# Optimization experiments

Measured on AMD Instinct MI355X. Metric: run time of the kernel, lower is better.

The kernel has to match this reference:

```python
import jax, jax.numpy as jnp
import numpy as np

B, S = 256, 16384
HUBER_DELTA = 1.0  # torch.nn.HuberLoss default


def setup_inputs() -> dict:
    key = jax.random.key(0)
    k1, k2, k3 = jax.random.split(key, 3)
    pred_coords = jax.random.normal(k1, (B, S, 3), dtype=jnp.float32)
    target_coords = jax.random.normal(k2, (B, S, 3), dtype=jnp.float32)
    mask = jax.random.randint(k3, (B, S), 0, 2).astype(jnp.int32)
    return {"pred_coords": pred_coords, "target_coords": target_coords, "mask": mask}


def _kabsch_align(pred, target, maskf):
    # pred/target: [B,S,3], maskf: [B,S] (0/1). Batched masked Kabsch.
    cnt = maskf.sum(axis=1, keepdims=True)                      # [B,1]
    cp = (pred * maskf[..., None]).sum(axis=1) / cnt            # [B,3] pred center
    ct = (target * maskf[..., None]).sum(axis=1) / cnt          # [B,3] target center
    pc = (pred - cp[:, None, :]) * maskf[..., None]             # masked centered pred
    tc = target - ct[:, None, :]                                # centered target
    H = jnp.einsum('bsi,bsj->bij', pc, tc)                      # [B,3,3] covariance
    U, _, Vt = jnp.linalg.svd(H)                                # batched 3x3 SVD
    R = jnp.einsum('bji,bkj->bik', Vt, U)                       # Vt^T @ U^T
    sign = jnp.where(jnp.linalg.det(R) < 0, -1.0, 1.0)          # [B] reflection fix
    flip = jnp.ones((pred.shape[0], 3), dtype=pred.dtype).at[:, -1].set(sign)
    Vt = Vt * flip[:, :, None]                                  # flip last row of Vt
    R = jnp.einsum('bji,bkj->bik', Vt, U)
    t = ct - jnp.einsum('bij,bj->bi', R, cp)                    # [B,3]
    aligned = jnp.einsum('bij,bsj->bsi', R, pred) + t[:, None, :]
    return aligned


def _huber(d):
    a = jnp.abs(d)
    return jnp.where(a < HUBER_DELTA, 0.5 * d * d, HUBER_DELTA * (a - 0.5 * HUBER_DELTA))


def reference(pred_coords, target_coords, mask):
    maskf = mask.astype(pred_coords.dtype)                      # [B,S]
    aligned = _kabsch_align(pred_coords, target_coords, maskf)  # [B,S,3]
    # (torch computes a clamped coord_diff here but never uses it in the loss)
    loss = _huber(aligned - target_coords) * maskf[..., None]   # [B,S,3]
    return loss.sum() / maskf.sum()
```

## Files before the change

kernel.cpp:

```cpp
#include <hip/hip_runtime.h>


#define NB 256
#define NS 16384
#define TPB 256
#define PB 8
#define SUB 2
#define PPT 4
#define NBLK (NB * PB)

__device__ __forceinline__ float wave_sum(float v) {
#pragma unroll
    for (int o = 32; o > 0; o >>= 1) v += __shfl_xor(v, o, 64);
    return v;
}

__device__ __forceinline__ float huber(float d) {
    float a = fabsf(d);
    return a < 1.f ? 0.5f * d * d : a - 0.5f;
}

__global__ __launch_bounds__(TPB) void reduce_kernel(
    const float* __restrict__ pred, const float* __restrict__ tgt,
    const int* __restrict__ mask, float* __restrict__ part)
{
    const int b = blockIdx.y, j = blockIdx.x, tid = threadIdx.x;
    float acc[16];
#pragma unroll
    for (int i = 0; i < 16; ++i) acc[i] = 0.f;
#pragma unroll
    for (int c = 0; c < SUB; ++c) {
        const long base = (long)b * NS + (long)j * (SUB * TPB * PPT)
                        + (long)c * (TPB * PPT) + (long)tid * PPT;
        const float4* p4 = reinterpret_cast<const float4*>(pred + base * 3);
        const float4* t4 = reinterpret_cast<const float4*>(tgt + base * 3);
        const int4 m4 = *reinterpret_cast<const int4*>(mask + base);
        float4 pA = p4[0], pB = p4[1], pC = p4[2];
        float4 tA = t4[0], tB = t4[1], tC = t4[2];
        float P[4][3] = {{pA.x,pA.y,pA.z},{pA.w,pB.x,pB.y},{pB.z,pB.w,pC.x},{pC.y,pC.z,pC.w}};
        float T[4][3] = {{tA.x,tA.y,tA.z},{tA.w,tB.x,tB.y},{tB.z,tB.w,tC.x},{tC.y,tC.z,tC.w}};
        float m[4] = {(float)m4.x,(float)m4.y,(float)m4.z,(float)m4.w};
#pragma unroll
        for (int k = 0; k < PPT; ++k) {
            const float mk = m[k];
            const float mp0 = mk * P[k][0], mp1 = mk * P[k][1], mp2 = mk * P[k][2];
            acc[0] += mk;
            acc[1] += mp0;            acc[2] += mp1;            acc[3] += mp2;
            acc[4] += mk * T[k][0];   acc[5] += mk * T[k][1];   acc[6] += mk * T[k][2];
            acc[7]  += mp0 * T[k][0]; acc[8]  += mp0 * T[k][1]; acc[9]  += mp0 * T[k][2];
            acc[10] += mp1 * T[k][0]; acc[11] += mp1 * T[k][1]; acc[12] += mp1 * T[k][2];
            acc[13] += mp2 * T[k][0]; acc[14] += mp2 * T[k][1]; acc[15] += mp2 * T[k][2];
        }
    }
#pragma unroll
    for (int i = 0; i < 16; ++i) acc[i] = wave_sum(acc[i]);

    __shared__ float red[4][16];
    const int wave = tid >> 6, lane = tid & 63;
    if (lane == 0) {
#pragma unroll
        for (int i = 0; i < 16; ++i) red[wave][i] = acc[i];
    }
    __syncthreads();
    if (tid < 16)
        part[((b * PB + j) << 4) + tid] =
            red[0][tid] + red[1][tid] + red[2][tid] + red[3][tid];
}

__global__ __launch_bounds__(NB) void svd_kernel(
    const float* __restrict__ part, float* __restrict__ RT)
{
    const int b = threadIdx.x;
    const float4* p4 = reinterpret_cast<const float4*>(part);
    float a[16];
#pragma unroll
    for (int i = 0; i < 16; ++i) a[i] = 0.f;
#pragma unroll
    for (int k = 0; k < PB; ++k) {
        const int row = (b * PB + k) << 2;
        float4 v0 = p4[row], v1 = p4[row+1], v2 = p4[row+2], v3 = p4[row+3];
        a[0]+=v0.x;  a[1]+=v0.y;  a[2]+=v0.z;  a[3]+=v0.w;
        a[4]+=v1.x;  a[5]+=v1.y;  a[6]+=v1.z;  a[7]+=v1.w;
        a[8]+=v2.x;  a[9]+=v2.y;  a[10]+=v2.z; a[11]+=v2.w;
        a[12]+=v3.x; a[13]+=v3.y; a[14]+=v3.z; a[15]+=v3.w;
    }
    const float cnt = a[0];
    const float inv = 1.f / cnt;
    const float cpx=a[1]*inv, cpy=a[2]*inv, cpz=a[3]*inv;
    const float ctx=a[4]*inv, cty=a[5]*inv, ctz=a[6]*inv;
    const float Sxx = a[7]  - cnt*cpx*ctx;
    const float Sxy = a[8]  - cnt*cpx*cty;
    const float Sxz = a[9]  - cnt*cpx*ctz;
    const float Syx = a[10] - cnt*cpy*ctx;
    const float Syy = a[11] - cnt*cpy*cty;
    const float Syz = a[12] - cnt*cpy*ctz;
    const float Szx = a[13] - cnt*cpz*ctx;
    const float Szy = a[14] - cnt*cpz*cty;
    const float Szz = a[15] - cnt*cpz*ctz;
    float N00 =  Sxx + Syy + Szz;
    float N01 =  Syz - Szy;
    float N02 =  Szx - Sxz;
    float N03 =  Sxy - Syx;
    float N11 =  Sxx - Syy - Szz;
    float N12 =  Sxy + Syx;
    float N13 =  Szx + Sxz;
    float N22 = -Sxx + Syy - Szz;
    float N23 =  Syz + Szy;
    float N33 = -Sxx - Syy + Szz;
    const float fro = sqrtf(N00*N00 + N11*N11 + N22*N22 + N33*N33 +
                2.f*(N01*N01 + N02*N02 + N03*N03 + N12*N12 + N13*N13 + N23*N23));
    const float isc = 1.f / (fro + 1e-30f);
    N00*=isc; N01*=isc; N02*=isc; N03*=isc; N11*=isc;
    N12*=isc; N13*=isc; N22*=isc; N23*=isc; N33*=isc;

    float qw = 1.f, qx = 0.1f, qy = 0.2f, qz = 0.3f;
    for (int it = 0; it < 160; ++it) {
        float nw = N00*qw + N01*qx + N02*qy + N03*qz + qw;
        float nx = N01*qw + N11*qx + N12*qy + N13*qz + qx;
        float ny = N02*qw + N12*qx + N22*qy + N23*qz + qy;
        float nz = N03*qw + N13*qx + N23*qy + N33*qz + qz;
        if ((it & 7) == 7) {
            const float r = rsqrtf(nw*nw + nx*nx + ny*ny + nz*nz);
            nw *= r; nx *= r; ny *= r; nz *= r;
        }
        qw = nw; qx = nx; qy = ny; qz = nz;
    }
    const float r = rsqrtf(qw*qw + qx*qx + qy*qy + qz*qz);
    qw *= r; qx *= r; qy *= r; qz *= r;
    const float R00 = 1.f - 2.f*(qy*qy + qz*qz);
    const float R01 = 2.f*(qx*qy - qw*qz);
    const float R02 = 2.f*(qx*qz + qw*qy);
    const float R10 = 2.f*(qx*qy + qw*qz);
    const float R11 = 1.f - 2.f*(qx*qx + qz*qz);
    const float R12 = 2.f*(qy*qz - qw*qx);
    const float R20 = 2.f*(qx*qz - qw*qy);
    const float R21 = 2.f*(qy*qz + qw*qx);
    const float R22 = 1.f - 2.f*(qx*qx + qy*qy);
    float* o = RT + b * 16;
    o[0]=R00; o[1]=R01; o[2]=R02; o[3]=R10; o[4]=R11; o[5]=R12;
    o[6]=R20; o[7]=R21; o[8]=R22;
    o[9]  = ctx - (R00*cpx + R01*cpy + R02*cpz);
    o[10] = cty - (R10*cpx + R11*cpy + R12*cpz);
    o[11] = ctz - (R20*cpx + R21*cpy + R22*cpz);
    o[12] = cnt;
}

__global__ __launch_bounds__(TPB) void loss_kernel(
    const float* __restrict__ pred, const float* __restrict__ tgt,
    const int* __restrict__ mask, const float* __restrict__ RT,
    float* __restrict__ lpart)
{
    const int b = blockIdx.y, j = blockIdx.x, tid = threadIdx.x;
    __shared__ float C[12];
    if (tid < 12) C[tid] = RT[b * 16 + tid];
    __syncthreads();
    float ls = 0.f;
#pragma unroll
    for (int c = 0; c < SUB; ++c) {
        const long base = (long)b * NS + (long)j * (SUB * TPB * PPT)
                        + (long)c * (TPB * PPT) + (long)tid * PPT;
        const float4* p4 = reinterpret_cast<const float4*>(pred + base * 3);
        const float4* t4 = reinterpret_cast<const float4*>(tgt + base * 3);
        const int4 m4 = *reinterpret_cast<const int4*>(mask + base);
        float4 pA = p4[0], pB = p4[1], pC = p4[2];
        float4 tA = t4[0], tB = t4[1], tC = t4[2];
        float P[4][3] = {{pA.x,pA.y,pA.z},{pA.w,pB.x,pB.y},{pB.z,pB.w,pC.x},{pC.y,pC.z,pC.w}};
        float T[4][3] = {{tA.x,tA.y,tA.z},{tA.w,tB.x,tB.y},{tB.z,tB.w,tC.x},{tC.y,tC.z,tC.w}};
        float m[4] = {(float)m4.x,(float)m4.y,(float)m4.z,(float)m4.w};
#pragma unroll
        for (int k = 0; k < PPT; ++k) {
            const float ax = C[0]*P[k][0] + C[1]*P[k][1] + C[2]*P[k][2] + C[9];
            const float ay = C[3]*P[k][0] + C[4]*P[k][1] + C[5]*P[k][2] + C[10];
            const float az = C[6]*P[k][0] + C[7]*P[k][1] + C[8]*P[k][2] + C[11];
            ls += m[k] * (huber(ax - T[k][0]) + huber(ay - T[k][1]) + huber(az - T[k][2]));
        }
    }
    ls = wave_sum(ls);
    __shared__ float red[4];
    const int wave = tid >> 6, lane = tid & 63;
    if (lane == 0) red[wave] = ls;
    __syncthreads();
    if (tid == 0) lpart[b * PB + j] = red[0] + red[1] + red[2] + red[3];
}

__global__ __launch_bounds__(NB) void final_kernel(
    const float* __restrict__ lpart, const float* __restrict__ RT,
    float* __restrict__ out)
{
    const int tid = threadIdx.x;
    float ls = 0.f;
#pragma unroll
    for (int k = 0; k < PB; ++k) ls += lpart[tid + NB * k];
    float cs = RT[tid * 16 + 12];
    ls = wave_sum(ls);
    cs = wave_sum(cs);
    __shared__ float rl[4], rc[4];
    const int wave = tid >> 6, lane = tid & 63;
    if (lane == 0) { rl[wave] = ls; rc[wave] = cs; }
    __syncthreads();
    if (tid == 0)
        out[0] = (rl[0]+rl[1]+rl[2]+rl[3]) / (rc[0]+rc[1]+rc[2]+rc[3]);
}

extern "C" void kernel_launch(void* const* d_in, const int* in_sizes, int n_in,
                              void* d_out, int out_size, void* d_ws, size_t ws_size,
                              hipStream_t stream) {
    const float* pred = (const float*)d_in[0];
    const float* tgt  = (const float*)d_in[1];
    const int*   mask = (const int*)d_in[2];
    float* out = (float*)d_out;

    float* part  = (float*)d_ws;
    float* RT    = part + NBLK * 16;
    float* lpart = RT + NB * 16;

    dim3 grid(PB, NB);
    reduce_kernel<<<grid, TPB, 0, stream>>>(pred, tgt, mask, part);
    svd_kernel<<<1, NB, 0, stream>>>(part, RT);
    loss_kernel<<<grid, TPB, 0, stream>>>(pred, tgt, mask, RT, lpart);
    final_kernel<<<1, NB, 0, stream>>>(lpart, RT, out);
}
```

Baseline: 169.0 us.

## Stage coalesced tile loads through LDS with two-half software pipelining

The reduce and loss kernels now load each 2048-point tile as fully coalesced float4 streams (consecutive threads read consecutive float4s) and stage them in shared memory. The tile is processed in two halves, with the second half's global loads issued before computing on the first. Previously each thread read three strided float4s per 4 points, so a wave's accesses were not contiguous. The change adds LDS traffic, extra barriers and about 28KB of shared memory per block, which may limit occupancy.

```diff
diff --git a/kernel.cpp b/kernel.cpp
--- a/kernel.cpp
+++ b/kernel.cpp
@@ -4,9 +4,9 @@
 #define NB 256
 #define NS 16384
 #define TPB 256
-#define PB 8
-#define SUB 2
-#define PPT 4
+#define TILE 2048
+#define HALF 1024
+#define PB (NS / TILE)
 #define NBLK (NB * PB)
 
 __device__ __forceinline__ float wave_sum(float v) {
@@ -20,51 +20,86 @@
     return a < 1.f ? 0.5f * d * d : a - 0.5f;
 }
 
-__global__ __launch_bounds__(TPB) void reduce_kernel(
+__global__ __launch_bounds__(TPB, 4) void reduce_kernel(
     const float* __restrict__ pred, const float* __restrict__ tgt,
     const int* __restrict__ mask, float* __restrict__ part)
 {
-    const int b = blockIdx.y, j = blockIdx.x, tid = threadIdx.x;
+    const int b = blockIdx.y, j = blockIdx.x, t = threadIdx.x;
+    const long pt0 = (long)b * NS + (long)j * TILE;
+    const float4* pf4 = reinterpret_cast<const float4*>(pred + pt0 * 3);
+    const float4* tf4 = reinterpret_cast<const float4*>(tgt + pt0 * 3);
+    const int4*   mi4 = reinterpret_cast<const int4*>(mask + pt0);
+
+    __shared__ float sP[HALF * 3];
+    __shared__ float sT[HALF * 3];
+    __shared__ int   sM[HALF];
+    float4* sP4 = reinterpret_cast<float4*>(sP);
+    float4* sT4 = reinterpret_cast<float4*>(sT);
+    int4*   sM4 = reinterpret_cast<int4*>(sM);
+
     float acc[16];
 #pragma unroll
     for (int i = 0; i < 16; ++i) acc[i] = 0.f;
-#pragma unroll
-    for (int c = 0; c < SUB; ++c) {
-        const long base = (long)b * NS + (long)j * (SUB * TPB * PPT)
-                        + (long)c * (TPB * PPT) + (long)tid * PPT;
-        const float4* p4 = reinterpret_cast<const float4*>(pred + base * 3);
-        const float4* t4 = reinterpret_cast<const float4*>(tgt + base * 3);
-        const int4 m4 = *reinterpret_cast<const int4*>(mask + base);
-        float4 pA = p4[0], pB = p4[1], pC = p4[2];
-        float4 tA = t4[0], tB = t4[1], tC = t4[2];
-        float P[4][3] = {{pA.x,pA.y,pA.z},{pA.w,pB.x,pB.y},{pB.z,pB.w,pC.x},{pC.y,pC.z,pC.w}};
-        float T[4][3] = {{tA.x,tA.y,tA.z},{tA.w,tB.x,tB.y},{tB.z,tB.w,tC.x},{tC.y,tC.z,tC.w}};
-        float m[4] = {(float)m4.x,(float)m4.y,(float)m4.z,(float)m4.w};
-#pragma unroll
-        for (int k = 0; k < PPT; ++k) {
-            const float mk = m[k];
-            const float mp0 = mk * P[k][0], mp1 = mk * P[k][1], mp2 = mk * P[k][2];
-            acc[0] += mk;
-            acc[1] += mp0;            acc[2] += mp1;            acc[3] += mp2;
-            acc[4] += mk * T[k][0];   acc[5] += mk * T[k][1];   acc[6] += mk * T[k][2];
-            acc[7]  += mp0 * T[k][0]; acc[8]  += mp0 * T[k][1]; acc[9]  += mp0 * T[k][2];
-            acc[10] += mp1 * T[k][0]; acc[11] += mp1 * T[k][1]; acc[12] += mp1 * T[k][2];
-            acc[13] += mp2 * T[k][0]; acc[14] += mp2 * T[k][1]; acc[15] += mp2 * T[k][2];
-        }
-    }
+
+    float4 gp0 = pf4[t], gp1 = pf4[t + 256], gp2 = pf4[t + 512];
+    float4 gt0 = tf4[t], gt1 = tf4[t + 256], gt2 = tf4[t + 512];
+    int4   gm  = mi4[t];
+    sP4[t] = gp0; sP4[t + 256] = gp1; sP4[t + 512] = gp2;
+    sT4[t] = gt0; sT4[t + 256] = gt1; sT4[t + 512] = gt2;
+    sM4[t] = gm;
+    __syncthreads();
+
+    float4 hp0 = pf4[768 + t], hp1 = pf4[1024 + t], hp2 = pf4[1280 + t];
+    float4 ht0 = tf4[768 + t], ht1 = tf4[1024 + t], ht2 = tf4[1280 + t];
+    int4   hm  = mi4[256 + t];
+
+#pragma unroll
+    for (int k = 0; k < 4; ++k) {
+        const int p = t + (k << 8);
+        const float mk = (float)sM[p];
+        const float px = sP[3*p], py = sP[3*p+1], pz = sP[3*p+2];
+        const float tx = sT[3*p], ty = sT[3*p+1], tz = sT[3*p+2];
+        const float mp0 = mk * px, mp1 = mk * py, mp2 = mk * pz;
+        acc[0] += mk;
+        acc[1] += mp0;       acc[2] += mp1;       acc[3] += mp2;
+        acc[4] += mk * tx;   acc[5] += mk * ty;   acc[6] += mk * tz;
+        acc[7]  += mp0 * tx; acc[8]  += mp0 * ty; acc[9]  += mp0 * tz;
+        acc[10] += mp1 * tx; acc[11] += mp1 * ty; acc[12] += mp1 * tz;
+        acc[13] += mp2 * tx; acc[14] += mp2 * ty; acc[15] += mp2 * tz;
+    }
+    __syncthreads();
+
+    sP4[t] = hp0; sP4[t + 256] = hp1; sP4[t + 512] = hp2;
+    sT4[t] = ht0; sT4[t + 256] = ht1; sT4[t + 512] = ht2;
+    sM4[t] = hm;
+    __syncthreads();
+#pragma unroll
+    for (int k = 0; k < 4; ++k) {
+        const int p = t + (k << 8);
+        const float mk = (float)sM[p];
+        const float px = sP[3*p], py = sP[3*p+1], pz = sP[3*p+2];
+        const float tx = sT[3*p], ty = sT[3*p+1], tz = sT[3*p+2];
+        const float mp0 = mk * px, mp1 = mk * py, mp2 = mk * pz;
+        acc[0] += mk;
+        acc[1] += mp0;       acc[2] += mp1;       acc[3] += mp2;
+        acc[4] += mk * tx;   acc[5] += mk * ty;   acc[6] += mk * tz;
+        acc[7]  += mp0 * tx; acc[8]  += mp0 * ty; acc[9]  += mp0 * tz;
+        acc[10] += mp1 * tx; acc[11] += mp1 * ty; acc[12] += mp1 * tz;
+        acc[13] += mp2 * tx; acc[14] += mp2 * ty; acc[15] += mp2 * tz;
+    }
+
 #pragma unroll
     for (int i = 0; i < 16; ++i) acc[i] = wave_sum(acc[i]);
-
     __shared__ float red[4][16];
-    const int wave = tid >> 6, lane = tid & 63;
+    const int wave = t >> 6, lane = t & 63;
     if (lane == 0) {
 #pragma unroll
         for (int i = 0; i < 16; ++i) red[wave][i] = acc[i];
     }
     __syncthreads();
-    if (tid < 16)
-        part[((b * PB + j) << 4) + tid] =
-            red[0][tid] + red[1][tid] + red[2][tid] + red[3][tid];
+    if (t < 16)
+        part[((b * PB + j) << 4) + t] =
+            red[0][t] + red[1][t] + red[2][t] + red[3][t];
 }
 
 __global__ __launch_bounds__(NB) void svd_kernel(
@@ -145,42 +180,75 @@
     o[12] = cnt;
 }
 
-__global__ __launch_bounds__(TPB) void loss_kernel(
+__global__ __launch_bounds__(TPB, 4) void loss_kernel(
     const float* __restrict__ pred, const float* __restrict__ tgt,
     const int* __restrict__ mask, const float* __restrict__ RT,
     float* __restrict__ lpart)
 {
-    const int b = blockIdx.y, j = blockIdx.x, tid = threadIdx.x;
+    const int b = blockIdx.y, j = blockIdx.x, t = threadIdx.x;
+    const long pt0 = (long)b * NS + (long)j * TILE;
+    const float4* pf4 = reinterpret_cast<const float4*>(pred + pt0 * 3);
+    const float4* tf4 = reinterpret_cast<const float4*>(tgt + pt0 * 3);
+    const int4*   mi4 = reinterpret_cast<const int4*>(mask + pt0);
+
+    __shared__ float sP[HALF * 3];
+    __shared__ float sT[HALF * 3];
+    __shared__ int   sM[HALF];
     __shared__ float C[12];
-    if (tid < 12) C[tid] = RT[b * 16 + tid];
-    __syncthreads();
+    float4* sP4 = reinterpret_cast<float4*>(sP);
+    float4* sT4 = reinterpret_cast<float4*>(sT);
+    int4*   sM4 = reinterpret_cast<int4*>(sM);
+
+    if (t < 12) C[t] = RT[b * 16 + t];
+
     float ls = 0.f;
-#pragma unroll
-    for (int c = 0; c < SUB; ++c) {
-        const long base = (long)b * NS + (long)j * (SUB * TPB * PPT)
-                        + (long)c * (TPB * PPT) + (long)tid * PPT;
-        const float4* p4 = reinterpret_cast<const float4*>(pred + base * 3);
-        const float4* t4 = reinterpret_cast<const float4*>(tgt + base * 3);
-        const int4 m4 = *reinterpret_cast<const int4*>(mask + base);
-        float4 pA = p4[0], pB = p4[1], pC = p4[2];
-        float4 tA = t4[0], tB = t4[1], tC = t4[2];
-        float P[4][3] = {{pA.x,pA.y,pA.z},{pA.w,pB.x,pB.y},{pB.z,pB.w,pC.x},{pC.y,pC.z,pC.w}};
-        float T[4][3] = {{tA.x,tA.y,tA.z},{tA.w,tB.x,tB.y},{tB.z,tB.w,tC.x},{tC.y,tC.z,tC.w}};
-        float m[4] = {(float)m4.x,(float)m4.y,(float)m4.z,(float)m4.w};
-#pragma unroll
-        for (int k = 0; k < PPT; ++k) {
-            const float ax = C[0]*P[k][0] + C[1]*P[k][1] + C[2]*P[k][2] + C[9];
-            const float ay = C[3]*P[k][0] + C[4]*P[k][1] + C[5]*P[k][2] + C[10];
-            const float az = C[6]*P[k][0] + C[7]*P[k][1] + C[8]*P[k][2] + C[11];
-            ls += m[k] * (huber(ax - T[k][0]) + huber(ay - T[k][1]) + huber(az - T[k][2]));
-        }
-    }
+    float4 gp0 = pf4[t], gp1 = pf4[t + 256], gp2 = pf4[t + 512];
+    float4 gt0 = tf4[t], gt1 = tf4[t + 256], gt2 = tf4[t + 512];
+    int4   gm  = mi4[t];
+    sP4[t] = gp0; sP4[t + 256] = gp1; sP4[t + 512] = gp2;
+    sT4[t] = gt0; sT4[t + 256] = gt1; sT4[t + 512] = gt2;
+    sM4[t] = gm;
+    __syncthreads();
+
+    float4 hp0 = pf4[768 + t], hp1 = pf4[1024 + t], hp2 = pf4[1280 + t];
+    float4 ht0 = tf4[768 + t], ht1 = tf4[1024 + t], ht2 = tf4[1280 + t];
+    int4   hm  = mi4[256 + t];
+
+#pragma unroll
+    for (int k = 0; k < 4; ++k) {
+        const int p = t + (k << 8);
+        const float mk = (float)sM[p];
+        const float px = sP[3*p], py = sP[3*p+1], pz = sP[3*p+2];
+        const float tx = sT[3*p], ty = sT[3*p+1], tz = sT[3*p+2];
+        const float ax = C[0]*px + C[1]*py + C[2]*pz + C[9];
+        const float ay = C[3]*px + C[4]*py + C[5]*pz + C[10];
+        const float az = C[6]*px + C[7]*py + C[8]*pz + C[11];
+        ls += mk * (huber(ax - tx) + huber(ay - ty) + huber(az - tz));
+    }
+    __syncthreads();
+
+    sP4[t] = hp0; sP4[t + 256] = hp1; sP4[t + 512] = hp2;
+    sT4[t] = ht0; sT4[t + 256] = ht1; sT4[t + 512] = ht2;
+    sM4[t] = hm;
+    __syncthreads();
+#pragma unroll
+    for (int k = 0; k < 4; ++k) {
+        const int p = t + (k << 8);
+        const float mk = (float)sM[p];
+        const float px = sP[3*p], py = sP[3*p+1], pz = sP[3*p+2];
+        const float tx = sT[3*p], ty = sT[3*p+1], tz = sT[3*p+2];
+        const float ax = C[0]*px + C[1]*py + C[2]*pz + C[9];
+        const float ay = C[3]*px + C[4]*py + C[5]*pz + C[10];
+        const float az = C[6]*px + C[7]*py + C[8]*pz + C[11];
+        ls += mk * (huber(ax - tx) + huber(ay - ty) + huber(az - tz));
+    }
+
     ls = wave_sum(ls);
     __shared__ float red[4];
-    const int wave = tid >> 6, lane = tid & 63;
+    const int wave = t >> 6, lane = t & 63;
     if (lane == 0) red[wave] = ls;
     __syncthreads();
-    if (tid == 0) lpart[b * PB + j] = red[0] + red[1] + red[2] + red[3];
+    if (t == 0) lpart[b * PB + j] = red[0] + red[1] + red[2] + red[3];
 }
 
 __global__ __launch_bounds__(NB) void final_kernel(
```

After: 170.0 us. Within noise of the previous version (+0.6%).
